# Optimization experiments

Measured on AMD Instinct MI355X. Metric: run time of the kernel, lower is better.

Reference implementation:

```python
import jax, jax.numpy as jnp
import numpy as np

D_MODEL = 1024
N_HEAD = 16
D_HEAD = D_MODEL // N_HEAD


def setup_inputs() -> dict:
    key = jax.random.key(0)
    k1, k2, k3 = jax.random.split(key, 3)
    x = jax.random.normal(k1, (4, 1024, D_MODEL), dtype=jnp.float32)
    # torch Linear(d_model, 3*d_model, bias=False): weight [3*d_model, d_model], y = x @ W.T
    w_qkv = jax.random.normal(k2, (3 * D_MODEL, D_MODEL), dtype=jnp.float32) * (1.0 / np.sqrt(D_MODEL))
    w_out = jax.random.normal(k3, (D_MODEL, D_MODEL), dtype=jnp.float32) * (1.0 / np.sqrt(D_MODEL))
    return {"x": x, "w_qkv": w_qkv, "w_out": w_out}


def reference(x, w_qkv, w_out):
    B, T, C = x.shape
    qkv = x @ w_qkv.T                                   # [B,T,3C]
    qkv = qkv.reshape(B, T, 3, N_HEAD, D_HEAD)
    q = jnp.transpose(qkv[:, :, 0], (0, 2, 1, 3))       # [B,H,T,Dh]
    k = jnp.transpose(qkv[:, :, 1], (0, 2, 1, 3))
    v = jnp.transpose(qkv[:, :, 2], (0, 2, 1, 3))
    att = jnp.einsum('bhqd,bhkd->bhqk', q, k) / jnp.sqrt(jnp.float32(D_HEAD))
    causal = jnp.tril(jnp.ones((T, T), dtype=bool))
    att = jnp.where(causal[None, None], att, -jnp.inf)
    att = jax.nn.softmax(att, axis=-1)
    y = jnp.einsum('bhqk,bhkd->bhqd', att, v)           # [B,H,T,Dh]
    y = jnp.transpose(y, (0, 2, 1, 3)).reshape(B, T, C)
    return y @ w_out.T
```

## Files before the change

kernel.cpp:

```cpp
#include <hip/hip_runtime.h>
#include <hip/hip_bf16.h>
#include <stdint.h>

#define DM 1024
#define NH 16
#define DH 64
#define BB 4
#define TT 1024
#define MR (BB*TT)

typedef __attribute__((ext_vector_type(8))) short bf16x8;
typedef __attribute__((ext_vector_type(4))) float f32x4;

typedef unsigned int __attribute__((address_space(1))) uint_g;
typedef unsigned int __attribute__((address_space(3))) uint_l;

static __device__ __forceinline__ void gload_lds16(const void* g, void* l) {
  __builtin_amdgcn_global_load_lds((const uint_g*)g, (uint_l*)l, 16, 0, 0);
}

static __device__ __forceinline__ unsigned short f2bf(float f) {
  union { float f; unsigned int u; } v; v.f = f;
  unsigned int r = v.u + 0x7fffu + ((v.u >> 16) & 1u);
  return (unsigned short)(r >> 16);
}
static __device__ __forceinline__ unsigned short f2bf_fast(float f) {
  union { float f; unsigned int u; } v; v.f = f;
  return (unsigned short)((v.u + 0x8000u) >> 16);
}

__global__ __launch_bounds__(256) void k_cvt3(const float* __restrict__ x,
    const float* __restrict__ w1, const float* __restrict__ w2,
    unsigned short* __restrict__ xb, unsigned short* __restrict__ wqb,
    unsigned short* __restrict__ wob) {
  const int n1 = (MR * DM) / 4, n2 = (3 * DM * DM) / 4, n3 = (DM * DM) / 4;
  const int total = n1 + n2 + n3;
  for (int u = blockIdx.x * 256 + threadIdx.x; u < total; u += gridDim.x * 256) {
    const float* src; unsigned short* dst; int i;
    if (u < n1)           { src = x;  dst = xb;  i = u; }
    else if (u < n1 + n2) { src = w1; dst = wqb; i = u - n1; }
    else                  { src = w2; dst = wob; i = u - n1 - n2; }
    float4 v = reinterpret_cast<const float4*>(src)[i];
    ushort4 o;
    o.x = f2bf(v.x); o.y = f2bf(v.y); o.z = f2bf(v.z); o.w = f2bf(v.w);
    reinterpret_cast<ushort4*>(dst)[i] = o;
  }
}

template<int EPI>
__global__ __launch_bounds__(256) void k_gemm(
    const unsigned short* __restrict__ A, const unsigned short* __restrict__ Bw,
    float* __restrict__ Of, unsigned short* __restrict__ qb,
    unsigned short* __restrict__ kb, unsigned short* __restrict__ vtb,
    int N, int K, int tiles_n) {
  __shared__ unsigned short SH[2][2][128 * 32];
  int tid = threadIdx.x;
  int w = tid >> 6, l = tid & 63;
  int l15 = l & 15, k8 = l >> 4;
  int nwg = gridDim.x;
  int cpx = nwg >> 3;
  int wg = blockIdx.x;
  int swz = (wg & 7) * cpx + (wg >> 3);
  int tm = swz / tiles_n, tn = swz % tiles_n;
  int m0 = tm << 7, n0 = tn << 7;

  f32x4 acc[4][4];
  #pragma unroll
  for (int i = 0; i < 4; ++i)
    #pragma unroll
    for (int j = 0; j < 4; ++j) acc[i][j] = (f32x4){0.f, 0.f, 0.f, 0.f};

  int srow = (w << 4) + (l >> 2);
  int sch = l & 3;
  int mrb = ((w >> 1) << 6) + l15;
  int nrb = ((w & 1) << 6) + l15;

  auto stage = [&](int buf, int kk) {
    #pragma unroll
    for (int p = 0; p < 2; ++p) {
      int row = srow + (p << 6);
      int c = sch ^ ((row >> 1) & 3);
      int seg = w + (p << 2);
      gload_lds16(A + (size_t)(m0 + row) * K + kk + (c << 3), &SH[buf][0][seg << 9]);
      gload_lds16(Bw + (size_t)(n0 + row) * K + kk + (c << 3), &SH[buf][1][seg << 9]);
    }
  };

  stage(0, 0);
  __syncthreads();
  int cur = 0;
  for (int kk = 0; kk < K; kk += 32) {
    if (kk + 32 < K) stage(cur ^ 1, kk + 32);
    bf16x8 a[4], b[4];
    #pragma unroll
    for (int mf = 0; mf < 4; ++mf) {
      int row = mrb + (mf << 4);
      a[mf] = *(const bf16x8*)&SH[cur][0][(row << 5) + ((k8 ^ ((row >> 1) & 3)) << 3)];
    }
    #pragma unroll
    for (int nf = 0; nf < 4; ++nf) {
      int row = nrb + (nf << 4);
      b[nf] = *(const bf16x8*)&SH[cur][1][(row << 5) + ((k8 ^ ((row >> 1) & 3)) << 3)];
    }
    #pragma unroll
    for (int mf = 0; mf < 4; ++mf)
      #pragma unroll
      for (int nf = 0; nf < 4; ++nf)
        acc[mf][nf] = __builtin_amdgcn_mfma_f32_16x16x32_bf16(a[mf], b[nf], acc[mf][nf], 0, 0, 0);
    __syncthreads();
    cur ^= 1;
  }

  if (EPI == 1) {
    #pragma unroll
    for (int mf = 0; mf < 4; ++mf)
      #pragma unroll
      for (int nf = 0; nf < 4; ++nf) {
        int n = n0 + ((w & 1) << 6) + (nf << 4) + l15;
        int m_base = m0 + ((w >> 1) << 6) + (mf << 4) + (k8 << 2);
        #pragma unroll
        for (int r = 0; r < 4; ++r)
          Of[(size_t)(m_base + r) * N + n] = acc[mf][nf][r];
      }
    return;
  }

  int s = n0 >> 10;
  if (s < 2) {
    #pragma unroll
    for (int mf = 0; mf < 4; ++mf) {
      #pragma unroll
      for (int nf = 0; nf < 4; ++nf) {
        int n = n0 + ((w & 1) << 6) + (nf << 4) + l15;
        int rem = n & 1023;
        int h = rem >> 6, d = rem & 63;
        int m_base = m0 + ((w >> 1) << 6) + (mf << 4) + (k8 << 2);
        #pragma unroll
        for (int r = 0; r < 4; ++r) {
          int m = m_base + r;
          int bb = m >> 10, t = m & 1023;
          float v = acc[mf][nf][r];
          if (s == 0)
            qb[((size_t)(bb * NH + h) * TT + t) * DH + d] = f2bf(v * 0.125f);
          else
            kb[((size_t)(bb * NH + h) * TT + t) * DH + d] = f2bf(v);
        }
      }
    }
  } else {
    unsigned short* T = &SH[0][0][0];
    int bb = m0 >> 10, t0 = m0 & 1023;
    int myhalf = w & 1;
    #pragma unroll
    for (int half = 0; half < 2; ++half) {
      __syncthreads();
      if (myhalf == half) {
        #pragma unroll
        for (int nf = 0; nf < 4; ++nf) {
          int nloc = (nf << 4) + l15;
          #pragma unroll
          for (int mf = 0; mf < 4; ++mf) {
            int mloc = ((w >> 1) << 6) + (mf << 4) + (k8 << 2);
            #pragma unroll
            for (int r = 0; r < 4; ++r)
              T[nloc * 134 + mloc + r] = f2bf(acc[mf][nf][r]);
          }
        }
      }
      __syncthreads();
      {
        int d = tid >> 2, mseg = tid & 3;
        int n = n0 + (half << 6) + d;
        int h = (n & 1023) >> 6;
        size_t base = ((size_t)(bb * NH + h) * DH + d) * TT + t0 + (mseg << 5);
        #pragma unroll
        for (int i = 0; i < 4; ++i) {
          ushort4 v4 = *(const ushort4*)&T[d * 134 + (mseg << 5) + (i << 3)];
          ushort4 v4b = *(const ushort4*)&T[d * 134 + (mseg << 5) + (i << 3) + 4];
          *(ushort4*)&vtb[base + (i << 3)] = v4;
          *(ushort4*)&vtb[base + (i << 3) + 4] = v4b;
        }
      }
    }
  }
}

__global__ __launch_bounds__(512) void k_attn(
    const unsigned short* __restrict__ qb, const unsigned short* __restrict__ kb,
    const unsigned short* __restrict__ vtb, unsigned short* __restrict__ yb) {
  __shared__ unsigned short Kt[2][64 * 64];
  __shared__ unsigned short Vt[2][64 * 64];
  __shared__ unsigned short Pl[8][16][72];
  int tid = threadIdx.x, w = tid >> 6, l = tid & 63;
  int l15 = l & 15, k8 = l >> 4;
  int bh = blockIdx.x >> 3;
  int a = blockIdx.x & 7;
  int wlo = w & 3;
  int qb_w = (w < 4) ? ((a << 6) + (wlo << 4))
                     : ((TT - ((a + 1) << 6)) + (wlo << 4));
  const unsigned short* Kb = kb + (size_t)bh * TT * DH;
  const unsigned short* Vb = vtb + (size_t)bh * DH * TT;
  const unsigned short* Qb = qb + (size_t)bh * TT * DH;

  int qrow = qb_w + l15;
  bf16x8 qf[2];
  #pragma unroll
  for (int c = 0; c < 2; ++c)
    qf[c] = *(const bf16x8*)&Qb[(size_t)qrow * DH + (c << 5) + (k8 << 3)];

  f32x4 y[4];
  #pragma unroll
  for (int i = 0; i < 4; ++i) y[i] = (f32x4){0.f, 0.f, 0.f, 0.f};
  float mrow = -INFINITY, lrow = 0.f;

  int srow = l >> 3;
  int sch = l & 7;

  auto stage = [&](int buf, int j0) {
    int row = (w << 3) + srow;
    int c = sch ^ (row & 7);
    gload_lds16(Kb + (size_t)(j0 + row) * DH + (c << 3), &Kt[buf][(w << 3) << 6]);
    gload_lds16(Vb + (size_t)row * TT + j0 + (c << 3), &Vt[buf][(w << 3) << 6]);
  };

  const int ns = 16 - a;
  stage(0, 0);
  __syncthreads();
  int cur = 0;

  for (int t = 0; t < ns; ++t) {
    int j0 = t << 6;
    if (t + 1 < ns) stage(cur ^ 1, (t + 1) << 6);

    if (j0 <= qb_w + 15) {
      f32x4 s[4];
      #pragma unroll
      for (int f = 0; f < 4; ++f) s[f] = (f32x4){0.f, 0.f, 0.f, 0.f};
      __builtin_amdgcn_s_setprio(1);
      #pragma unroll
      for (int c = 0; c < 2; ++c) {
        #pragma unroll
        for (int f = 0; f < 4; ++f) {
          int row = (f << 4) + l15;
          bf16x8 ak = *(const bf16x8*)&Kt[cur][(row << 6) + ((((c << 2) + k8) ^ (row & 7)) << 3)];
          s[f] = __builtin_amdgcn_mfma_f32_16x16x32_bf16(ak, qf[c], s[f], 0, 0, 0);
        }
      }
      __builtin_amdgcn_s_setprio(0);

      if (j0 + 64 > qb_w) {
        #pragma unroll
        for (int f = 0; f < 4; ++f)
          #pragma unroll
          for (int r = 0; r < 4; ++r)
            if (j0 + (f << 4) + (k8 << 2) + r > qrow) s[f][r] = -INFINITY;
      }

      float pmax = -INFINITY;
      #pragma unroll
      for (int f = 0; f < 4; ++f)
        #pragma unroll
        for (int r = 0; r < 4; ++r) pmax = fmaxf(pmax, s[f][r]);
      pmax = fmaxf(pmax, __shfl_xor(pmax, 16, 64));
      pmax = fmaxf(pmax, __shfl_xor(pmax, 32, 64));

      bool skip = __all(pmax - mrow <= 8.0f);
      float mnew = skip ? mrow : fmaxf(mrow, pmax);
      float psum = 0.f;
      #pragma unroll
      for (int f = 0; f < 4; ++f)
        #pragma unroll
        for (int r = 0; r < 4; ++r) {
          float p = __expf(s[f][r] - mnew);
          s[f][r] = p;
          psum += p;
        }
      psum += __shfl_xor(psum, 16, 64);
      psum += __shfl_xor(psum, 32, 64);
      if (!skip) {
        float alpha = __expf(mrow - mnew);
        lrow *= alpha;
        #pragma unroll
        for (int mf = 0; mf < 4; ++mf) y[mf] *= alpha;
        mrow = mnew;
      }
      lrow += psum;

      #pragma unroll
      for (int f = 0; f < 4; ++f) {
        ushort4 pk;
        pk.x = f2bf_fast(s[f][0]); pk.y = f2bf_fast(s[f][1]);
        pk.z = f2bf_fast(s[f][2]); pk.w = f2bf_fast(s[f][3]);
        *(ushort4*)&Pl[w][l15][(f << 4) + (k8 << 2)] = pk;
      }
      asm volatile("s_waitcnt lgkmcnt(0)" ::: "memory");
      __builtin_amdgcn_sched_barrier(0);

      __builtin_amdgcn_s_setprio(1);
      #pragma unroll
      for (int c = 0; c < 2; ++c) {
        bf16x8 bp = *(const bf16x8*)&Pl[w][l15][(c << 5) + (k8 << 3)];
        #pragma unroll
        for (int mf = 0; mf < 4; ++mf) {
          int dr = (mf << 4) + l15;
          bf16x8 av = *(const bf16x8*)&Vt[cur][(dr << 6) + ((((c << 2) + k8) ^ (dr & 7)) << 3)];
          y[mf] = __builtin_amdgcn_mfma_f32_16x16x32_bf16(av, bp, y[mf], 0, 0, 0);
        }
      }
      __builtin_amdgcn_s_setprio(0);
    }

    __syncthreads();
    cur ^= 1;
  }

  float inv = 1.f / lrow;
  int bb = bh >> 4, h = bh & 15;
  #pragma unroll
  for (int mf = 0; mf < 4; ++mf) {
    ushort4 o;
    o.x = f2bf(y[mf][0] * inv);
    o.y = f2bf(y[mf][1] * inv);
    o.z = f2bf(y[mf][2] * inv);
    o.w = f2bf(y[mf][3] * inv);
    *(ushort4*)&yb[((size_t)(bb * TT + qrow) << 10) + (h << 6) + (mf << 4) + (k8 << 2)] = o;
  }
}

extern "C" void kernel_launch(void* const* d_in, const int* in_sizes, int n_in,
                              void* d_out, int out_size, void* d_ws, size_t ws_size,
                              hipStream_t stream) {
  const float* x    = (const float*)d_in[0];
  const float* wqkv = (const float*)d_in[1];
  const float* wout = (const float*)d_in[2];
  char* ws = (char*)d_ws;
  unsigned short* xb  = (unsigned short*)(ws + (size_t)0);
  unsigned short* wqb = (unsigned short*)(ws + ((size_t)8  << 20));
  unsigned short* wob = (unsigned short*)(ws + ((size_t)14 << 20));
  unsigned short* qbv = (unsigned short*)(ws + ((size_t)16 << 20));
  unsigned short* kbv = (unsigned short*)(ws + ((size_t)24 << 20));
  unsigned short* vtb = (unsigned short*)(ws + ((size_t)32 << 20));
  unsigned short* yb  = (unsigned short*)(ws + ((size_t)40 << 20));

  k_cvt3<<<2048, 256, 0, stream>>>(x, wqkv, wout, xb, wqb, wob);
  k_gemm<0><<<768, 256, 0, stream>>>(xb, wqb, nullptr, qbv, kbv, vtb, 3 * DM, DM, 24);
  k_attn<<<512, 512, 0, stream>>>(qbv, kbv, vtb, yb);
  k_gemm<1><<<256, 256, 0, stream>>>(yb, wob, (float*)d_out, nullptr, nullptr, nullptr, DM, DM, 8);
}
```

Before: 96.06 us.

## Widen attention key tiles to 128, single-buffer V, split output GEMM tiles

The attention kernel now processes 128-key blocks per iteration. K is double-buffered and V is single-buffered, with V loaded at the start of each iteration and gated by a vmcnt wait plus a barrier before the PV step. This halves the number of loop iterations and barriers but raises register use (s[8]) and LDS footprint, and a launch-bounds occupancy hint is added. The output projection GEMM is split into its own kernel with 64x128 tiles and 512 blocks, so it fills more CUs than the previous 256-block launch. The QKV GEMM is specialised with constant sizes.

```diff
diff --git a/kernel.cpp b/kernel.cpp
--- a/kernel.cpp
+++ b/kernel.cpp
@@ -18,6 +18,8 @@
 static __device__ __forceinline__ void gload_lds16(const void* g, void* l) {
   __builtin_amdgcn_global_load_lds((const uint_g*)g, (uint_l*)l, 16, 0, 0);
 }
+
+static __device__ __forceinline__ void fence() { asm volatile("" ::: "memory"); }
 
 static __device__ __forceinline__ unsigned short f2bf(float f) {
   union { float f; unsigned int u; } v; v.f = f;
@@ -47,20 +49,17 @@
   }
 }
 
-template<int EPI>
-__global__ __launch_bounds__(256) void k_gemm(
+__global__ __launch_bounds__(256) void k_gemm0(
     const unsigned short* __restrict__ A, const unsigned short* __restrict__ Bw,
-    float* __restrict__ Of, unsigned short* __restrict__ qb,
-    unsigned short* __restrict__ kb, unsigned short* __restrict__ vtb,
-    int N, int K, int tiles_n) {
+    unsigned short* __restrict__ qb, unsigned short* __restrict__ kb,
+    unsigned short* __restrict__ vtb) {
+  const int K = DM, tiles_n = 24;
   __shared__ unsigned short SH[2][2][128 * 32];
   int tid = threadIdx.x;
   int w = tid >> 6, l = tid & 63;
   int l15 = l & 15, k8 = l >> 4;
-  int nwg = gridDim.x;
-  int cpx = nwg >> 3;
   int wg = blockIdx.x;
-  int swz = (wg & 7) * cpx + (wg >> 3);
+  int swz = (wg & 7) * 96 + (wg >> 3);
   int tm = swz / tiles_n, tn = swz % tiles_n;
   int m0 = tm << 7, n0 = tn << 7;
 
@@ -109,20 +108,6 @@
         acc[mf][nf] = __builtin_amdgcn_mfma_f32_16x16x32_bf16(a[mf], b[nf], acc[mf][nf], 0, 0, 0);
     __syncthreads();
     cur ^= 1;
-  }
-
-  if (EPI == 1) {
-    #pragma unroll
-    for (int mf = 0; mf < 4; ++mf)
-      #pragma unroll
-      for (int nf = 0; nf < 4; ++nf) {
-        int n = n0 + ((w & 1) << 6) + (nf << 4) + l15;
-        int m_base = m0 + ((w >> 1) << 6) + (mf << 4) + (k8 << 2);
-        #pragma unroll
-        for (int r = 0; r < 4; ++r)
-          Of[(size_t)(m_base + r) * N + n] = acc[mf][nf][r];
-      }
-    return;
   }
 
   int s = n0 >> 10;
@@ -185,11 +170,87 @@
   }
 }
 
-__global__ __launch_bounds__(512) void k_attn(
+__global__ __launch_bounds__(256) void k_gemm1(
+    const unsigned short* __restrict__ A, const unsigned short* __restrict__ Bw,
+    float* __restrict__ Of) {
+  const int N = DM, K = DM;
+  __shared__ unsigned short At[2][64 * 32];
+  __shared__ unsigned short Bt[2][128 * 32];
+  int tid = threadIdx.x;
+  int w = tid >> 6, l = tid & 63;
+  int l15 = l & 15, k8 = l >> 4;
+  int wg = blockIdx.x;
+  int swz = (wg & 7) * 64 + (wg >> 3);
+  int tm = swz >> 3, tn = swz & 7;
+  int m0 = tm << 6, n0 = tn << 7;
+  int wm = w >> 1, wn = w & 1;
+
+  f32x4 acc[2][4];
+  #pragma unroll
+  for (int i = 0; i < 2; ++i)
+    #pragma unroll
+    for (int j = 0; j < 4; ++j) acc[i][j] = (f32x4){0.f, 0.f, 0.f, 0.f};
+
+  int srl = l >> 2;
+  int sch = l & 3;
+
+  auto stage = [&](int buf, int kk) {
+    {
+      int row = (w << 4) + srl;
+      int c = sch ^ ((row >> 1) & 3);
+      gload_lds16(A + (size_t)(m0 + row) * K + kk + (c << 3), &At[buf][w << 9]);
+    }
+    #pragma unroll
+    for (int p = 0; p < 2; ++p) {
+      int seg = (w << 1) + p;
+      int row = (seg << 4) + srl;
+      int c = sch ^ ((row >> 1) & 3);
+      gload_lds16(Bw + (size_t)(n0 + row) * K + kk + (c << 3), &Bt[buf][seg << 9]);
+    }
+  };
+
+  stage(0, 0);
+  __syncthreads();
+  int cur = 0;
+  for (int kk = 0; kk < K; kk += 32) {
+    if (kk + 32 < K) stage(cur ^ 1, kk + 32);
+    bf16x8 a[2], b[4];
+    #pragma unroll
+    for (int mf = 0; mf < 2; ++mf) {
+      int row = (wm << 5) + (mf << 4) + l15;
+      a[mf] = *(const bf16x8*)&At[cur][(row << 5) + ((k8 ^ ((row >> 1) & 3)) << 3)];
+    }
+    #pragma unroll
+    for (int nf = 0; nf < 4; ++nf) {
+      int row = (wn << 6) + (nf << 4) + l15;
+      b[nf] = *(const bf16x8*)&Bt[cur][(row << 5) + ((k8 ^ ((row >> 1) & 3)) << 3)];
+    }
+    #pragma unroll
+    for (int mf = 0; mf < 2; ++mf)
+      #pragma unroll
+      for (int nf = 0; nf < 4; ++nf)
+        acc[mf][nf] = __builtin_amdgcn_mfma_f32_16x16x32_bf16(a[mf], b[nf], acc[mf][nf], 0, 0, 0);
+    __syncthreads();
+    cur ^= 1;
+  }
+
+  #pragma unroll
+  for (int mf = 0; mf < 2; ++mf)
+    #pragma unroll
+    for (int nf = 0; nf < 4; ++nf) {
+      int n = n0 + (wn << 6) + (nf << 4) + l15;
+      int m_base = m0 + (wm << 5) + (mf << 4) + (k8 << 2);
+      #pragma unroll
+      for (int r = 0; r < 4; ++r)
+        Of[(size_t)(m_base + r) * N + n] = acc[mf][nf][r];
+    }
+}
+
+__global__ __launch_bounds__(512, 4) void k_attn(
     const unsigned short* __restrict__ qb, const unsigned short* __restrict__ kb,
     const unsigned short* __restrict__ vtb, unsigned short* __restrict__ yb) {
-  __shared__ unsigned short Kt[2][64 * 64];
-  __shared__ unsigned short Vt[2][64 * 64];
+  __shared__ unsigned short Kt[2][128 * 64];
+  __shared__ unsigned short Vt[64 * 128];
   __shared__ unsigned short Pl[8][16][72];
   int tid = threadIdx.x, w = tid >> 6, l = tid & 63;
   int l15 = l & 15, k8 = l >> 4;
@@ -213,34 +274,45 @@
   for (int i = 0; i < 4; ++i) y[i] = (f32x4){0.f, 0.f, 0.f, 0.f};
   float mrow = -INFINITY, lrow = 0.f;
 
-  int srow = l >> 3;
-  int sch = l & 7;
-
-  auto stage = [&](int buf, int j0) {
-    int row = (w << 3) + srow;
-    int c = sch ^ (row & 7);
-    gload_lds16(Kb + (size_t)(j0 + row) * DH + (c << 3), &Kt[buf][(w << 3) << 6]);
-    gload_lds16(Vb + (size_t)row * TT + j0 + (c << 3), &Vt[buf][(w << 3) << 6]);
+  auto stageK = [&](int buf, int j0) {
+    #pragma unroll
+    for (int p = 0; p < 2; ++p) {
+      int base = (w << 4) + (p << 3);
+      int row = base + (l >> 3);
+      int c = (l & 7) ^ (row & 7);
+      gload_lds16(Kb + (size_t)(j0 + row) * DH + (c << 3), &Kt[buf][base << 6]);
+    }
   };
-
-  const int ns = 16 - a;
-  stage(0, 0);
+  auto stageV = [&](int j0) {
+    #pragma unroll
+    for (int p = 0; p < 2; ++p) {
+      int base = (w << 3) + (p << 2);
+      int row = base + (l >> 4);
+      int c = (l & 15) ^ (row & 7);
+      gload_lds16(Vb + (size_t)row * TT + j0 + (c << 3), &Vt[base << 7]);
+    }
+  };
+
+  const int ns = (17 - a) >> 1;
+  stageK(0, 0);
   __syncthreads();
   int cur = 0;
 
   for (int t = 0; t < ns; ++t) {
-    int j0 = t << 6;
-    if (t + 1 < ns) stage(cur ^ 1, (t + 1) << 6);
-
-    if (j0 <= qb_w + 15) {
-      f32x4 s[4];
-      #pragma unroll
-      for (int f = 0; f < 4; ++f) s[f] = (f32x4){0.f, 0.f, 0.f, 0.f};
+    int j0 = t << 7;
+    stageV(j0);
+    if (t + 1 < ns) stageK(cur ^ 1, j0 + 128);
+    bool active = (j0 <= qb_w + 15);
+
+    f32x4 s[8];
+    if (active) {
+      #pragma unroll
+      for (int f = 0; f < 8; ++f) s[f] = (f32x4){0.f, 0.f, 0.f, 0.f};
       __builtin_amdgcn_s_setprio(1);
       #pragma unroll
       for (int c = 0; c < 2; ++c) {
         #pragma unroll
-        for (int f = 0; f < 4; ++f) {
+        for (int f = 0; f < 8; ++f) {
           int row = (f << 4) + l15;
           bf16x8 ak = *(const bf16x8*)&Kt[cur][(row << 6) + ((((c << 2) + k8) ^ (row & 7)) << 3)];
           s[f] = __builtin_amdgcn_mfma_f32_16x16x32_bf16(ak, qf[c], s[f], 0, 0, 0);
@@ -248,9 +320,9 @@
       }
       __builtin_amdgcn_s_setprio(0);
 
-      if (j0 + 64 > qb_w) {
-        #pragma unroll
-        for (int f = 0; f < 4; ++f)
+      if (j0 + 128 > qb_w) {
+        #pragma unroll
+        for (int f = 0; f < 8; ++f)
           #pragma unroll
           for (int r = 0; r < 4; ++r)
             if (j0 + (f << 4) + (k8 << 2) + r > qrow) s[f][r] = -INFINITY;
@@ -258,7 +330,7 @@
 
       float pmax = -INFINITY;
       #pragma unroll
-      for (int f = 0; f < 4; ++f)
+      for (int f = 0; f < 8; ++f)
         #pragma unroll
         for (int r = 0; r < 4; ++r) pmax = fmaxf(pmax, s[f][r]);
       pmax = fmaxf(pmax, __shfl_xor(pmax, 16, 64));
@@ -268,7 +340,7 @@
       float mnew = skip ? mrow : fmaxf(mrow, pmax);
       float psum = 0.f;
       #pragma unroll
-      for (int f = 0; f < 4; ++f)
+      for (int f = 0; f < 8; ++f)
         #pragma unroll
         for (int r = 0; r < 4; ++r) {
           float p = __expf(s[f][r] - mnew);
@@ -285,29 +357,39 @@
         mrow = mnew;
       }
       lrow += psum;
-
-      #pragma unroll
-      for (int f = 0; f < 4; ++f) {
-        ushort4 pk;
-        pk.x = f2bf_fast(s[f][0]); pk.y = f2bf_fast(s[f][1]);
-        pk.z = f2bf_fast(s[f][2]); pk.w = f2bf_fast(s[f][3]);
-        *(ushort4*)&Pl[w][l15][(f << 4) + (k8 << 2)] = pk;
-      }
-      asm volatile("s_waitcnt lgkmcnt(0)" ::: "memory");
-      __builtin_amdgcn_sched_barrier(0);
-
-      __builtin_amdgcn_s_setprio(1);
-      #pragma unroll
-      for (int c = 0; c < 2; ++c) {
-        bf16x8 bp = *(const bf16x8*)&Pl[w][l15][(c << 5) + (k8 << 3)];
-        #pragma unroll
-        for (int mf = 0; mf < 4; ++mf) {
-          int dr = (mf << 4) + l15;
-          bf16x8 av = *(const bf16x8*)&Vt[cur][(dr << 6) + ((((c << 2) + k8) ^ (dr & 7)) << 3)];
-          y[mf] = __builtin_amdgcn_mfma_f32_16x16x32_bf16(av, bp, y[mf], 0, 0, 0);
-        }
-      }
-      __builtin_amdgcn_s_setprio(0);
+    }
+
+    if (t + 1 < ns) { asm volatile("s_waitcnt vmcnt(2)" ::: "memory"); }
+    else            { asm volatile("s_waitcnt vmcnt(0)" ::: "memory"); }
+    fence(); __builtin_amdgcn_s_barrier(); fence();
+
+    if (active) {
+      #pragma unroll
+      for (int h = 0; h < 2; ++h) {
+        #pragma unroll
+        for (int f4 = 0; f4 < 4; ++f4) {
+          f32x4 sv = s[(h << 2) + f4];
+          ushort4 pk;
+          pk.x = f2bf_fast(sv[0]); pk.y = f2bf_fast(sv[1]);
+          pk.z = f2bf_fast(sv[2]); pk.w = f2bf_fast(sv[3]);
+          *(ushort4*)&Pl[w][l15][(f4 << 4) + (k8 << 2)] = pk;
+        }
+        asm volatile("s_waitcnt lgkmcnt(0)" ::: "memory");
+        __builtin_amdgcn_sched_barrier(0);
+        __builtin_amdgcn_s_setprio(1);
+        #pragma unroll
+        for (int c2 = 0; c2 < 2; ++c2) {
+          bf16x8 bp = *(const bf16x8*)&Pl[w][l15][(c2 << 5) + (k8 << 3)];
+          int c = (h << 1) + c2;
+          #pragma unroll
+          for (int mf = 0; mf < 4; ++mf) {
+            int dr = (mf << 4) + l15;
+            bf16x8 av = *(const bf16x8*)&Vt[(dr << 7) + ((((c << 2) + k8) ^ (dr & 7)) << 3)];
+            y[mf] = __builtin_amdgcn_mfma_f32_16x16x32_bf16(av, bp, y[mf], 0, 0, 0);
+          }
+        }
+        __builtin_amdgcn_s_setprio(0);
+      }
     }
 
     __syncthreads();
@@ -343,7 +425,7 @@
   unsigned short* yb  = (unsigned short*)(ws + ((size_t)40 << 20));
 
   k_cvt3<<<2048, 256, 0, stream>>>(x, wqkv, wout, xb, wqb, wob);
-  k_gemm<0><<<768, 256, 0, stream>>>(xb, wqb, nullptr, qbv, kbv, vtb, 3 * DM, DM, 24);
+  k_gemm0<<<768, 256, 0, stream>>>(xb, wqb, qbv, kbv, vtb);
   k_attn<<<512, 512, 0, stream>>>(qbv, kbv, vtb, yb);
-  k_gemm<1><<<256, 256, 0, stream>>>(yb, wob, (float*)d_out, nullptr, nullptr, nullptr, DM, DM, 8);
-}
+  k_gemm1<<<512, 256, 0, stream>>>(yb, wob, (float*)d_out);
+}
```

New measurement: 102.2 us. 6.4% more time.
